# Optimization experiments

Measured on AMD Instinct MI355X. Metric: run time of the kernel, lower is better.

## Reference

```python
import jax, jax.numpy as jnp
import numpy as np

N_NODES = 50000
N_EDGES = 1600000
N_FEAT = 128
DROPOUT = 0.1


def setup_inputs() -> dict:
    key = jax.random.key(0)
    k1, k2, k3, k4 = jax.random.split(key, 4)
    x = jax.random.normal(k1, (N_NODES, N_FEAT), dtype=jnp.float32)
    adj_vals = jax.random.uniform(k2, (N_EDGES,), dtype=jnp.float32)
    row = jax.random.randint(k3, (N_EDGES,), 0, N_NODES, dtype=jnp.int32)
    col = jax.random.randint(k4, (N_EDGES,), 0, N_NODES, dtype=jnp.int32)
    return {"x": x, "adj_vals": adj_vals, "row": row, "col": col}


def reference(x, adj_vals, row, col):
    # MixedDropout on sparse adjacency values (deterministic fixed key),
    # then SpMM: out[i] = sum_{e: row[e]==i} A_drop[e] * x[col[e]]
    keep_prob = 1.0 - DROPOUT
    mask_key = jax.random.fold_in(jax.random.key(42), 7)
    keep = jax.random.bernoulli(mask_key, keep_prob, adj_vals.shape)
    vals_drop = jnp.where(keep, adj_vals / keep_prob, 0.0)
    # gather source features and weight by (dropped) edge values
    msgs = vals_drop[:, None] * x[col]  # [E, F]
    out = jax.ops.segment_sum(msgs, row, num_segments=N_NODES)  # [N, F]
    return out
```

## Files before the change

kernel.cpp:

```cpp
#include <hip/hip_runtime.h>
#include <stdint.h>

#define N_NODES 50000
#define N_EDGES 1600000
#define N_FEAT 128
#define CAP 64
#define OVF_PW 256
#define OVF_PB 192

#define RSHIFT 7
#define BROWS 128
#define NB 391
#define NWG_A 250
#define A_THREADS 1024
#define CHUNKS_PW 1600
#define CAPW 40
#define NREG (NWG_A + NB)


struct KeyPair { uint32_t a, b; };

__host__ __device__ constexpr inline uint32_t rotl32(uint32_t x, int r) {
  return (x << r) | (x >> (32 - r));
}

__host__ __device__ constexpr inline KeyPair threefry2x32(uint32_t k0, uint32_t k1,
                                                          uint32_t x0, uint32_t x1) {
  const uint32_t ks0 = k0, ks1 = k1, ks2 = k0 ^ k1 ^ 0x1BD11BDAu;
  x0 += ks0;
  x1 += ks1;
  const int rotA[4] = {13, 15, 26, 6};
  const int rotB[4] = {17, 29, 16, 24};
  const uint32_t ks[3] = {ks0, ks1, ks2};
  for (int i = 0; i < 5; ++i) {
    const int* rot = (i & 1) ? rotB : rotA;
    for (int j = 0; j < 4; ++j) {
      x0 += x1;
      x1 = rotl32(x1, rot[j]);
      x1 ^= x0;
    }
    x0 += ks[(i + 1) % 3];
    x1 += ks[(i + 2) % 3] + (uint32_t)(i + 1);
  }
  return {x0, x1};
}

constexpr KeyPair MASK_KEY = threefry2x32(0u, 42u, 0u, 7u);

__device__ inline bool edge_keep(uint32_t e) {
  KeyPair r = threefry2x32(MASK_KEY.a, MASK_KEY.b, 0u, e);
  uint32_t bits = r.a ^ r.b;
  float u = __uint_as_float((bits >> 9) | 0x3f800000u) - 1.0f;
  return u < 0.9f;
}

__device__ inline uint32_t f2bf(uint32_t b) {
  return (b + 0x7fffu + ((b >> 16) & 1u)) >> 16;
}

typedef uint32_t u4v __attribute__((ext_vector_type(4)));
typedef int32_t  i4v __attribute__((ext_vector_type(4)));
typedef float    f4v __attribute__((ext_vector_type(4)));


__global__ void __launch_bounds__(A_THREADS) convA_kernel(const float* __restrict__ x,
                                                          uint32_t* __restrict__ xb,
                                                          const float* __restrict__ adj_vals,
                                                          const int* __restrict__ row,
                                                          const int* __restrict__ col,
                                                          uint64_t* __restrict__ coarse,
                                                          uint32_t* __restrict__ lens,
                                                          uint32_t* __restrict__ ovfcA,
                                                          uint64_t* __restrict__ ovfA) {
  __shared__ uint32_t cnt[NB];
  __shared__ uint32_t ovfc;
  int wg = blockIdx.x;
  int tid = threadIdx.x;
  if (tid < NB) cnt[tid] = 0;
  if (tid == 0) ovfc = 0;

  const int gthreads = NWG_A * A_THREADS;
  for (int i = wg * A_THREADS + tid; i < (N_NODES * N_FEAT) / 8; i += gthreads) {
    f4v a = __builtin_nontemporal_load((const f4v*)x + 2 * i);
    f4v b = __builtin_nontemporal_load((const f4v*)x + 2 * i + 1);
    u4v o;
    o.x = f2bf(__float_as_uint(a.x)) | (f2bf(__float_as_uint(a.y)) << 16);
    o.y = f2bf(__float_as_uint(a.z)) | (f2bf(__float_as_uint(a.w)) << 16);
    o.z = f2bf(__float_as_uint(b.x)) | (f2bf(__float_as_uint(b.y)) << 16);
    o.w = f2bf(__float_as_uint(b.z)) | (f2bf(__float_as_uint(b.w)) << 16);
    ((u4v*)xb)[i] = o;
  }
  __syncthreads();

  uint64_t* my_coarse = coarse + (size_t)wg * NB * CAPW;
  for (int ch = tid; ch < CHUNKS_PW; ch += A_THREADS) {
    const int g = wg * CHUNKS_PW + ch;
    const i4v r4 = __builtin_nontemporal_load((const i4v*)row + g);
    const i4v c4 = __builtin_nontemporal_load((const i4v*)col + g);
    const f4v a4 = __builtin_nontemporal_load((const f4v*)adj_vals + g);
    const int rr[4] = {r4.x, r4.y, r4.z, r4.w};
    const int cc[4] = {c4.x, c4.y, c4.z, c4.w};
    const float aa[4] = {a4.x, a4.y, a4.z, a4.w};
#pragma unroll
    for (int k = 0; k < 4; ++k) {
      const uint32_t e = (uint32_t)(4 * g + k);
      if (!edge_keep(e)) continue;
      const uint32_t r = (uint32_t)rr[k];
      const uint32_t c = (uint32_t)cc[k];
      const float v = aa[k] / 0.9f;
      const uint32_t b = r >> RSHIFT;
      const uint32_t li = atomicAdd(&cnt[b], 1u);
      const uint64_t p = ((uint64_t)r << 48) | ((uint64_t)c << 32) | (uint64_t)__float_as_uint(v);
      if (li < CAPW) {
        my_coarse[(size_t)b * CAPW + li] = p;
      } else {
        const uint32_t oi = atomicAdd(&ovfc, 1u);
        if (oi < OVF_PW) ovfA[(size_t)wg * OVF_PW + oi] = p;
      }
    }
  }
  __syncthreads();
  if (tid < NB) lens[(size_t)tid * NWG_A + wg] = min(cnt[tid], (uint32_t)CAPW);
  if (tid == 0) ovfcA[wg] = min(ovfc, (uint32_t)OVF_PW);
}

__global__ void __launch_bounds__(512) rank_gather_kernel(const uint32_t* __restrict__ xb,
                                                          const uint64_t* __restrict__ coarse,
                                                          const uint32_t* __restrict__ lens,
                                                          uint32_t* __restrict__ ovfcB,
                                                          uint64_t* __restrict__ ovfB,
                                                          float* __restrict__ out) {
  int b = blockIdx.x;
  int tid = threadIdx.x;
  __shared__ uint32_t pay[BROWS * CAP];
  __shared__ uint32_t cnt[BROWS];
  __shared__ uint32_t s_len[NWG_A];
  __shared__ uint32_t ovfc;
  for (int i = tid; i < BROWS * CAP; i += 512) pay[i] = 0u;
  if (tid < BROWS) cnt[tid] = 0;
  if (tid < NWG_A) s_len[tid] = lens[(size_t)b * NWG_A + tid];
  if (tid == 0) ovfc = 0;
  __syncthreads();

  int team = tid >> 4;
  int lane = tid & 15;

  uint32_t lenv[8];
  uint64_t pre[8];
#pragma unroll
  for (int s8 = 0; s8 < 8; ++s8) {
    int seg = team + (s8 << 5);
    lenv[s8] = (seg < NWG_A) ? s_len[seg] : 0u;
    pre[s8] = (seg < NWG_A)
        ? __builtin_nontemporal_load(coarse + ((size_t)seg * NB + b) * CAPW + lane)
        : 0ull;
  }
  uint64_t tl[8];
#pragma unroll
  for (int s8 = 0; s8 < 8; ++s8) {
    int seg = team + (s8 << 5);
    tl[s8] = (lenv[s8] > 16u && (uint32_t)(lane + 16) < lenv[s8])
        ? __builtin_nontemporal_load(coarse + ((size_t)seg * NB + b) * CAPW + 16 + lane)
        : 0ull;
  }

#define RANK(p)                                                              \
  {                                                                          \
    uint32_t r = (uint32_t)((p) >> 48);                                      \
    uint32_t rl = r & (BROWS - 1);                                           \
    uint32_t idx = atomicAdd(&cnt[rl], 1u);                                  \
    if (idx < CAP) {                                                         \
      uint32_t c = (uint32_t)((p) >> 32) & 0xFFFFu;                          \
      pay[rl * CAP + idx] = (c << 16) | f2bf((uint32_t)(p));                 \
    } else {                                                                 \
      uint32_t oi = atomicAdd(&ovfc, 1u);                                    \
      if (oi < OVF_PB) ovfB[(size_t)b * OVF_PB + oi] = (p);                  \
    }                                                                        \
  }

#pragma unroll
  for (int s8 = 0; s8 < 8; ++s8) {
    if ((uint32_t)lane < lenv[s8]) RANK(pre[s8]);
  }
#pragma unroll
  for (int s8 = 0; s8 < 8; ++s8) {
    if (lenv[s8] > 16u && (uint32_t)(lane + 16) < lenv[s8]) RANK(tl[s8]);
  }
#pragma unroll
  for (int s8 = 0; s8 < 8; ++s8) {
    uint32_t len = lenv[s8];
    if (len > 32u) {
      int seg = team + (s8 << 5);
      const uint64_t* cseg = coarse + ((size_t)seg * NB + b) * CAPW;
      for (uint32_t li = 32u + (uint32_t)lane; li < len; li += 16) {
        uint64_t p = __builtin_nontemporal_load(cseg + li);
        RANK(p);
      }
    }
  }
#undef RANK
  __syncthreads();
  if (tid == 0) ovfcB[b] = min(ovfc, (uint32_t)OVF_PB);

  const uint4* x4 = (const uint4*)xb;
  const int r0 = b << RSHIFT;

#define GSTEP(ww)                                                            \
  {                                                                          \
    uint32_t cc = (ww) >> 16;                                                \
    float vv = __uint_as_float((ww) << 16);                                  \
    uint4 a = x4[(size_t)cc * 16 + lane];                                    \
    acc0 += vv * __uint_as_float(a.x << 16);                                 \
    acc1 += vv * __uint_as_float(a.x & 0xffff0000u);                         \
    acc2 += vv * __uint_as_float(a.y << 16);                                 \
    acc3 += vv * __uint_as_float(a.y & 0xffff0000u);                         \
    acc4 += vv * __uint_as_float(a.z << 16);                                 \
    acc5 += vv * __uint_as_float(a.z & 0xffff0000u);                         \
    acc6 += vv * __uint_as_float(a.w << 16);                                 \
    acc7 += vv * __uint_as_float(a.w & 0xffff0000u);                         \
  }

  for (int rl = team; rl < BROWS; rl += 32) {
    int r = r0 + rl;
    if (r >= N_NODES) continue;
    uint32_t n = (min(cnt[rl], (uint32_t)CAP) + 7u) & ~7u;
    const uint32_t* prow = &pay[rl * CAP];
    float acc0 = 0.f, acc1 = 0.f, acc2 = 0.f, acc3 = 0.f;
    float acc4 = 0.f, acc5 = 0.f, acc6 = 0.f, acc7 = 0.f;
    for (uint32_t j = 0; j < n; j += 8) {
      uint32_t w0 = prow[j + 0];
      uint32_t w1 = prow[j + 1];
      uint32_t w2 = prow[j + 2];
      uint32_t w3 = prow[j + 3];
      uint32_t w4 = prow[j + 4];
      uint32_t w5 = prow[j + 5];
      uint32_t w6 = prow[j + 6];
      uint32_t w7 = prow[j + 7];
      GSTEP(w0) GSTEP(w1) GSTEP(w2) GSTEP(w3)
      GSTEP(w4) GSTEP(w5) GSTEP(w6) GSTEP(w7)
    }
    f4v lo, hi;
    lo.x = acc0; lo.y = acc1; lo.z = acc2; lo.w = acc3;
    hi.x = acc4; hi.y = acc5; hi.z = acc6; hi.w = acc7;
    f4v* o = (f4v*)out + (size_t)r * 32 + lane * 2;
    __builtin_nontemporal_store(lo, o);
    __builtin_nontemporal_store(hi, o + 1);
  }
#undef GSTEP
}

__global__ void __launch_bounds__(256) ovf_pack_kernel(const float* __restrict__ x,
                                                       const uint32_t* __restrict__ ovfcA,
                                                       const uint64_t* __restrict__ ovfA,
                                                       const uint32_t* __restrict__ ovfcB,
                                                       const uint64_t* __restrict__ ovfB,
                                                       float* __restrict__ out) {
  __shared__ int any;
  if (threadIdx.x == 0) any = 0;
  __syncthreads();
  for (int t = threadIdx.x; t < NREG; t += 256) {
    uint32_t c = (t < NWG_A) ? ovfcA[t] : ovfcB[t - NWG_A];
    if (c) any = 1;
  }
  __syncthreads();
  if (!any) return;

  int group = (int)((blockIdx.x * 256 + threadIdx.x) >> 7);
  int f = threadIdx.x & 127;
  const int ngroups = (16 * 256) >> 7;
  for (int reg = group; reg < NREG; reg += ngroups) {
    uint32_t c;
    const uint64_t* basep;
    if (reg < NWG_A) {
      c = min(ovfcA[reg], (uint32_t)OVF_PW);
      basep = ovfA + (size_t)reg * OVF_PW;
    } else {
      c = min(ovfcB[reg - NWG_A], (uint32_t)OVF_PB);
      basep = ovfB + (size_t)(reg - NWG_A) * OVF_PB;
    }
    for (uint32_t i = 0; i < c; ++i) {
      uint64_t p = basep[i];
      uint32_t r = (uint32_t)(p >> 48);
      uint32_t cc = (uint32_t)((p >> 32) & 0xFFFFu);
      float v = __uint_as_float((uint32_t)p);
      atomicAdd(&out[(size_t)r * N_FEAT + f], v * x[(size_t)cc * N_FEAT + f]);
    }
  }
}


__global__ void __launch_bounds__(256) scatter_fused_kernel(const float* __restrict__ x,
                                                            const float* __restrict__ adj_vals,
                                                            const int* __restrict__ row,
                                                            const int* __restrict__ col,
                                                            float* __restrict__ out) {
  long long t = (long long)blockIdx.x * blockDim.x + threadIdx.x;
  int e = (int)(t >> 6);
  int lane = (int)(t & 63);
  if (e >= N_EDGES) return;
  if (!edge_keep((uint32_t)e)) return;
  float v = adj_vals[e] / 0.9f;
  float2 xf = *(const float2*)(x + (long long)col[e] * N_FEAT + lane * 2);
  float* dst = out + (long long)row[e] * N_FEAT + lane * 2;
  atomicAdd(dst, v * xf.x);
  atomicAdd(dst + 1, v * xf.y);
}


extern "C" void kernel_launch(void* const* d_in, const int* in_sizes, int n_in,
                              void* d_out, int out_size, void* d_ws, size_t ws_size,
                              hipStream_t stream) {
  const float* x        = (const float*)d_in[0];
  const float* adj_vals = (const float*)d_in[1];
  const int*   row      = (const int*)d_in[2];
  const int*   col      = (const int*)d_in[3];
  float* out = (float*)d_out;

  size_t a_ovfcA   = 0;
  size_t a_ovfcB   = (a_ovfcA + (size_t)NWG_A * 4 + 255) & ~255ull;
  size_t a_lens    = (a_ovfcB + (size_t)NB * 4 + 255) & ~255ull;
  size_t a_ovfA    = (a_lens + (size_t)NB * NWG_A * 4 + 255) & ~255ull;
  size_t a_ovfB    = (a_ovfA + (size_t)NWG_A * OVF_PW * 8 + 255) & ~255ull;
  size_t a_coarse  = (a_ovfB + (size_t)NB * OVF_PB * 8 + 255) & ~255ull;
  size_t a_xb      = (a_coarse + (size_t)NWG_A * NB * CAPW * 8 + 255) & ~255ull;
  size_t need      = a_xb + (size_t)N_NODES * N_FEAT * 2;

  if (ws_size >= need) {
    uint32_t* ovfcA   = (uint32_t*)((char*)d_ws + a_ovfcA);
    uint32_t* ovfcB   = (uint32_t*)((char*)d_ws + a_ovfcB);
    uint32_t* lens    = (uint32_t*)((char*)d_ws + a_lens);
    uint64_t* ovfA    = (uint64_t*)((char*)d_ws + a_ovfA);
    uint64_t* ovfB    = (uint64_t*)((char*)d_ws + a_ovfB);
    uint64_t* coarse  = (uint64_t*)((char*)d_ws + a_coarse);
    uint32_t* xb      = (uint32_t*)((char*)d_ws + a_xb);

    convA_kernel<<<NWG_A, A_THREADS, 0, stream>>>(x, xb, adj_vals, row, col,
                                                  coarse, lens, ovfcA, ovfA);
    rank_gather_kernel<<<NB, 512, 0, stream>>>(xb, coarse, lens, ovfcB, ovfB, out);
    ovf_pack_kernel<<<16, 256, 0, stream>>>(x, ovfcA, ovfA, ovfcB, ovfB, out);
  } else {
    hipMemsetAsync(d_out, 0, (size_t)out_size * sizeof(float), stream);
    long long total_threads = (long long)N_EDGES * 64;
    scatter_fused_kernel<<<(int)((total_threads + 255) / 256), 256, 0, stream>>>(
        x, adj_vals, row, col, out);
  }
}
```

Measured before the change: 152.1 us.

## Split coarse bucket records into packed payload and row-local byte arrays

The binning pass now writes each edge as a 32-bit packed column/bf16 value word plus a separate 8-bit local row index, instead of one 64-bit record. The bf16 conversion moves out of the ranking kernel, which shrinks both the intermediate write and its later re-read. The ranking kernel also rotates slot indices by the local row to spread LDS bank accesses, and the overflow buffer becomes 32-bit with a repacked encoding. The extra byte-array loads are narrow and may coalesce poorly, and the sync moved ahead of the x conversion loop changes where the block waits.

```diff
diff --git a/kernel.cpp b/kernel.cpp
--- a/kernel.cpp
+++ b/kernel.cpp
@@ -68,7 +68,8 @@
                                                           const float* __restrict__ adj_vals,
                                                           const int* __restrict__ row,
                                                           const int* __restrict__ col,
-                                                          uint64_t* __restrict__ coarse,
+                                                          uint32_t* __restrict__ cpay,
+                                                          uint8_t* __restrict__ crl,
                                                           uint32_t* __restrict__ lens,
                                                           uint32_t* __restrict__ ovfcA,
                                                           uint64_t* __restrict__ ovfA) {
@@ -78,6 +79,7 @@
   int tid = threadIdx.x;
   if (tid < NB) cnt[tid] = 0;
   if (tid == 0) ovfc = 0;
+  __syncthreads();
 
   const int gthreads = NWG_A * A_THREADS;
   for (int i = wg * A_THREADS + tid; i < (N_NODES * N_FEAT) / 8; i += gthreads) {
@@ -90,9 +92,9 @@
     o.w = f2bf(__float_as_uint(b.z)) | (f2bf(__float_as_uint(b.w)) << 16);
     ((u4v*)xb)[i] = o;
   }
-  __syncthreads();
-
-  uint64_t* my_coarse = coarse + (size_t)wg * NB * CAPW;
+
+  uint32_t* my_pay = cpay + (size_t)wg * NB * CAPW;
+  uint8_t* my_rl = crl + (size_t)wg * NB * CAPW;
   for (int ch = tid; ch < CHUNKS_PW; ch += A_THREADS) {
     const int g = wg * CHUNKS_PW + ch;
     const i4v r4 = __builtin_nontemporal_load((const i4v*)row + g);
@@ -110,12 +112,15 @@
       const float v = aa[k] / 0.9f;
       const uint32_t b = r >> RSHIFT;
       const uint32_t li = atomicAdd(&cnt[b], 1u);
-      const uint64_t p = ((uint64_t)r << 48) | ((uint64_t)c << 32) | (uint64_t)__float_as_uint(v);
       if (li < CAPW) {
-        my_coarse[(size_t)b * CAPW + li] = p;
+        const size_t off = (size_t)b * CAPW + li;
+        my_pay[off] = (c << 16) | f2bf(__float_as_uint(v));
+        my_rl[off] = (uint8_t)(r & (BROWS - 1));
       } else {
         const uint32_t oi = atomicAdd(&ovfc, 1u);
-        if (oi < OVF_PW) ovfA[(size_t)wg * OVF_PW + oi] = p;
+        if (oi < OVF_PW)
+          ovfA[(size_t)wg * OVF_PW + oi] =
+              ((uint64_t)r << 48) | ((uint64_t)c << 32) | (uint64_t)__float_as_uint(v);
       }
     }
   }
@@ -125,10 +130,11 @@
 }
 
 __global__ void __launch_bounds__(512) rank_gather_kernel(const uint32_t* __restrict__ xb,
-                                                          const uint64_t* __restrict__ coarse,
+                                                          const uint32_t* __restrict__ cpay,
+                                                          const uint8_t* __restrict__ crl,
                                                           const uint32_t* __restrict__ lens,
                                                           uint32_t* __restrict__ ovfcB,
-                                                          uint64_t* __restrict__ ovfB,
+                                                          uint32_t* __restrict__ ovfB,
                                                           float* __restrict__ out) {
   int b = blockIdx.x;
   int tid = threadIdx.x;
@@ -146,55 +152,56 @@
   int lane = tid & 15;
 
   uint32_t lenv[8];
-  uint64_t pre[8];
+  uint32_t pw[8];
+  uint32_t prl[8];
 #pragma unroll
   for (int s8 = 0; s8 < 8; ++s8) {
     int seg = team + (s8 << 5);
     lenv[s8] = (seg < NWG_A) ? s_len[seg] : 0u;
-    pre[s8] = (seg < NWG_A)
-        ? __builtin_nontemporal_load(coarse + ((size_t)seg * NB + b) * CAPW + lane)
-        : 0ull;
-  }
-  uint64_t tl[8];
+    size_t off = ((size_t)seg * NB + b) * CAPW + lane;
+    pw[s8] = (seg < NWG_A) ? __builtin_nontemporal_load(cpay + off) : 0u;
+    prl[s8] = (seg < NWG_A) ? (uint32_t)__builtin_nontemporal_load(crl + off) : 0u;
+  }
+  uint32_t tw[8];
+  uint32_t trl[8];
 #pragma unroll
   for (int s8 = 0; s8 < 8; ++s8) {
     int seg = team + (s8 << 5);
-    tl[s8] = (lenv[s8] > 16u && (uint32_t)(lane + 16) < lenv[s8])
-        ? __builtin_nontemporal_load(coarse + ((size_t)seg * NB + b) * CAPW + 16 + lane)
-        : 0ull;
-  }
-
-#define RANK(p)                                                              \
+    bool tv = (lenv[s8] > 16u && (uint32_t)(lane + 16) < lenv[s8]);
+    size_t off = ((size_t)seg * NB + b) * CAPW + 16 + lane;
+    tw[s8] = tv ? __builtin_nontemporal_load(cpay + off) : 0u;
+    trl[s8] = tv ? (uint32_t)__builtin_nontemporal_load(crl + off) : 0u;
+  }
+
+#define RANK(w, rl)                                                          \
   {                                                                          \
-    uint32_t r = (uint32_t)((p) >> 48);                                      \
-    uint32_t rl = r & (BROWS - 1);                                           \
-    uint32_t idx = atomicAdd(&cnt[rl], 1u);                                  \
+    uint32_t idx = atomicAdd(&cnt[(rl)], 1u);                                \
     if (idx < CAP) {                                                         \
-      uint32_t c = (uint32_t)((p) >> 32) & 0xFFFFu;                          \
-      pay[rl * CAP + idx] = (c << 16) | f2bf((uint32_t)(p));                 \
+      pay[(rl) * CAP + ((idx + (rl)) & (CAP - 1))] = (w);                    \
     } else {                                                                 \
       uint32_t oi = atomicAdd(&ovfc, 1u);                                    \
-      if (oi < OVF_PB) ovfB[(size_t)b * OVF_PB + oi] = (p);                  \
+      if (oi < OVF_PB) ovfB[(size_t)b * OVF_PB + oi] = ((rl) << 24) | ((w) >> 8) | (((w) & 0xFFu) << 16); \
     }                                                                        \
   }
 
 #pragma unroll
   for (int s8 = 0; s8 < 8; ++s8) {
-    if ((uint32_t)lane < lenv[s8]) RANK(pre[s8]);
-  }
-#pragma unroll
-  for (int s8 = 0; s8 < 8; ++s8) {
-    if (lenv[s8] > 16u && (uint32_t)(lane + 16) < lenv[s8]) RANK(tl[s8]);
+    if ((uint32_t)lane < lenv[s8]) RANK(pw[s8], prl[s8]);
+  }
+#pragma unroll
+  for (int s8 = 0; s8 < 8; ++s8) {
+    if (lenv[s8] > 16u && (uint32_t)(lane + 16) < lenv[s8]) RANK(tw[s8], trl[s8]);
   }
 #pragma unroll
   for (int s8 = 0; s8 < 8; ++s8) {
     uint32_t len = lenv[s8];
     if (len > 32u) {
       int seg = team + (s8 << 5);
-      const uint64_t* cseg = coarse + ((size_t)seg * NB + b) * CAPW;
+      size_t sbase = ((size_t)seg * NB + b) * CAPW;
       for (uint32_t li = 32u + (uint32_t)lane; li < len; li += 16) {
-        uint64_t p = __builtin_nontemporal_load(cseg + li);
-        RANK(p);
+        uint32_t w = __builtin_nontemporal_load(cpay + sbase + li);
+        uint32_t rl = (uint32_t)__builtin_nontemporal_load(crl + sbase + li);
+        RANK(w, rl);
       }
     }
   }
@@ -228,14 +235,14 @@
     float acc0 = 0.f, acc1 = 0.f, acc2 = 0.f, acc3 = 0.f;
     float acc4 = 0.f, acc5 = 0.f, acc6 = 0.f, acc7 = 0.f;
     for (uint32_t j = 0; j < n; j += 8) {
-      uint32_t w0 = prow[j + 0];
-      uint32_t w1 = prow[j + 1];
-      uint32_t w2 = prow[j + 2];
-      uint32_t w3 = prow[j + 3];
-      uint32_t w4 = prow[j + 4];
-      uint32_t w5 = prow[j + 5];
-      uint32_t w6 = prow[j + 6];
-      uint32_t w7 = prow[j + 7];
+      uint32_t w0 = prow[(j + 0 + rl) & (CAP - 1)];
+      uint32_t w1 = prow[(j + 1 + rl) & (CAP - 1)];
+      uint32_t w2 = prow[(j + 2 + rl) & (CAP - 1)];
+      uint32_t w3 = prow[(j + 3 + rl) & (CAP - 1)];
+      uint32_t w4 = prow[(j + 4 + rl) & (CAP - 1)];
+      uint32_t w5 = prow[(j + 5 + rl) & (CAP - 1)];
+      uint32_t w6 = prow[(j + 6 + rl) & (CAP - 1)];
+      uint32_t w7 = prow[(j + 7 + rl) & (CAP - 1)];
       GSTEP(w0) GSTEP(w1) GSTEP(w2) GSTEP(w3)
       GSTEP(w4) GSTEP(w5) GSTEP(w6) GSTEP(w7)
     }
@@ -253,13 +260,13 @@
                                                        const uint32_t* __restrict__ ovfcA,
                                                        const uint64_t* __restrict__ ovfA,
                                                        const uint32_t* __restrict__ ovfcB,
-                                                       const uint64_t* __restrict__ ovfB,
+                                                       const uint32_t* __restrict__ ovfB,
                                                        float* __restrict__ out) {
   __shared__ int any;
   if (threadIdx.x == 0) any = 0;
   __syncthreads();
   for (int t = threadIdx.x; t < NREG; t += 256) {
-    uint32_t c = (t < NWG_A) ? ovfcA[t] : ovfcB[t - NWG_A];
+    uint32_t c = (t < NWG_A) ? ovfcA[t] : ovfcB ? ((t - NWG_A < NB) ? ovfcB[t - NWG_A] : 0u) : 0u;
     if (c) any = 1;
   }
   __syncthreads();
@@ -269,21 +276,29 @@
   int f = threadIdx.x & 127;
   const int ngroups = (16 * 256) >> 7;
   for (int reg = group; reg < NREG; reg += ngroups) {
-    uint32_t c;
-    const uint64_t* basep;
     if (reg < NWG_A) {
-      c = min(ovfcA[reg], (uint32_t)OVF_PW);
-      basep = ovfA + (size_t)reg * OVF_PW;
+      uint32_t c = min(ovfcA[reg], (uint32_t)OVF_PW);
+      const uint64_t* basep = ovfA + (size_t)reg * OVF_PW;
+      for (uint32_t i = 0; i < c; ++i) {
+        uint64_t p = basep[i];
+        uint32_t r = (uint32_t)(p >> 48);
+        uint32_t cc = (uint32_t)((p >> 32) & 0xFFFFu);
+        float v = __uint_as_float((uint32_t)p);
+        atomicAdd(&out[(size_t)r * N_FEAT + f], v * x[(size_t)cc * N_FEAT + f]);
+      }
     } else {
-      c = min(ovfcB[reg - NWG_A], (uint32_t)OVF_PB);
-      basep = ovfB + (size_t)(reg - NWG_A) * OVF_PB;
-    }
-    for (uint32_t i = 0; i < c; ++i) {
-      uint64_t p = basep[i];
-      uint32_t r = (uint32_t)(p >> 48);
-      uint32_t cc = (uint32_t)((p >> 32) & 0xFFFFu);
-      float v = __uint_as_float((uint32_t)p);
-      atomicAdd(&out[(size_t)r * N_FEAT + f], v * x[(size_t)cc * N_FEAT + f]);
+      int bb = reg - NWG_A;
+      uint32_t c = min(ovfcB[bb], (uint32_t)OVF_PB);
+      const uint32_t* basep = ovfB + (size_t)bb * OVF_PB;
+      for (uint32_t i = 0; i < c; ++i) {
+        uint32_t s = basep[i];
+        uint32_t rl = s >> 24;
+        uint32_t w = ((s & 0x00FFFFu) << 8) | ((s >> 16) & 0xFFu);
+        uint32_t r = ((uint32_t)bb << RSHIFT) + rl;
+        uint32_t cc = w >> 16;
+        float v = __uint_as_float(w << 16);
+        atomicAdd(&out[(size_t)r * N_FEAT + f], v * x[(size_t)cc * N_FEAT + f]);
+      }
     }
   }
 }
@@ -321,22 +336,24 @@
   size_t a_lens    = (a_ovfcB + (size_t)NB * 4 + 255) & ~255ull;
   size_t a_ovfA    = (a_lens + (size_t)NB * NWG_A * 4 + 255) & ~255ull;
   size_t a_ovfB    = (a_ovfA + (size_t)NWG_A * OVF_PW * 8 + 255) & ~255ull;
-  size_t a_coarse  = (a_ovfB + (size_t)NB * OVF_PB * 8 + 255) & ~255ull;
-  size_t a_xb      = (a_coarse + (size_t)NWG_A * NB * CAPW * 8 + 255) & ~255ull;
+  size_t a_cpay    = (a_ovfB + (size_t)NB * OVF_PB * 4 + 255) & ~255ull;
+  size_t a_crl     = (a_cpay + (size_t)NWG_A * NB * CAPW * 4 + 255) & ~255ull;
+  size_t a_xb      = (a_crl + (size_t)NWG_A * NB * CAPW + 255) & ~255ull;
   size_t need      = a_xb + (size_t)N_NODES * N_FEAT * 2;
 
   if (ws_size >= need) {
-    uint32_t* ovfcA   = (uint32_t*)((char*)d_ws + a_ovfcA);
-    uint32_t* ovfcB   = (uint32_t*)((char*)d_ws + a_ovfcB);
-    uint32_t* lens    = (uint32_t*)((char*)d_ws + a_lens);
-    uint64_t* ovfA    = (uint64_t*)((char*)d_ws + a_ovfA);
-    uint64_t* ovfB    = (uint64_t*)((char*)d_ws + a_ovfB);
-    uint64_t* coarse  = (uint64_t*)((char*)d_ws + a_coarse);
-    uint32_t* xb      = (uint32_t*)((char*)d_ws + a_xb);
+    uint32_t* ovfcA = (uint32_t*)((char*)d_ws + a_ovfcA);
+    uint32_t* ovfcB = (uint32_t*)((char*)d_ws + a_ovfcB);
+    uint32_t* lens  = (uint32_t*)((char*)d_ws + a_lens);
+    uint64_t* ovfA  = (uint64_t*)((char*)d_ws + a_ovfA);
+    uint32_t* ovfB  = (uint32_t*)((char*)d_ws + a_ovfB);
+    uint32_t* cpay  = (uint32_t*)((char*)d_ws + a_cpay);
+    uint8_t*  crl   = (uint8_t*)((char*)d_ws + a_crl);
+    uint32_t* xb    = (uint32_t*)((char*)d_ws + a_xb);
 
     convA_kernel<<<NWG_A, A_THREADS, 0, stream>>>(x, xb, adj_vals, row, col,
-                                                  coarse, lens, ovfcA, ovfA);
-    rank_gather_kernel<<<NB, 512, 0, stream>>>(xb, coarse, lens, ovfcB, ovfB, out);
+                                                  cpay, crl, lens, ovfcA, ovfA);
+    rank_gather_kernel<<<NB, 512, 0, stream>>>(xb, cpay, crl, lens, ovfcB, ovfB, out);
     ovf_pack_kernel<<<16, 256, 0, stream>>>(x, ovfcA, ovfA, ovfcB, ovfB, out);
   } else {
     hipMemsetAsync(d_out, 0, (size_t)out_size * sizeof(float), stream);
```

After: 158.1 us. +4.0%, slower.

## Halve row buckets to 64 rows, rotate LDS slots, move barrier earlier

Applied to the files above, without the earlier changes.

Buckets now cover 64 rows instead of 128, which doubles the number of rank/gather workgroups, shrinks each workgroup to 256 threads and shrinks the per-workgroup coarse capacity and overflow budget. The LDS payload slot index is rotated by the row index so concurrent reads and writes across teams spread over banks. The barrier in convA now sits right after the shared counters are cleared, so the bf16 conversion loop and edge bucketing are no longer separated by a sync. The aim is more parallelism and less LDS per block. The smaller per-bucket capacity may push more edges to the overflow path.

```diff
diff --git a/kernel.cpp b/kernel.cpp
--- a/kernel.cpp
+++ b/kernel.cpp
@@ -6,15 +6,15 @@
 #define N_FEAT 128
 #define CAP 64
 #define OVF_PW 256
-#define OVF_PB 192
-
-#define RSHIFT 7
-#define BROWS 128
-#define NB 391
+#define OVF_PB 128
+
+#define RSHIFT 6
+#define BROWS 64
+#define NB 782
 #define NWG_A 250
 #define A_THREADS 1024
 #define CHUNKS_PW 1600
-#define CAPW 40
+#define CAPW 24
 #define NREG (NWG_A + NB)
 
 
@@ -78,6 +78,7 @@
   int tid = threadIdx.x;
   if (tid < NB) cnt[tid] = 0;
   if (tid == 0) ovfc = 0;
+  __syncthreads();
 
   const int gthreads = NWG_A * A_THREADS;
   for (int i = wg * A_THREADS + tid; i < (N_NODES * N_FEAT) / 8; i += gthreads) {
@@ -90,7 +91,6 @@
     o.w = f2bf(__float_as_uint(b.z)) | (f2bf(__float_as_uint(b.w)) << 16);
     ((u4v*)xb)[i] = o;
   }
-  __syncthreads();
 
   uint64_t* my_coarse = coarse + (size_t)wg * NB * CAPW;
   for (int ch = tid; ch < CHUNKS_PW; ch += A_THREADS) {
@@ -124,7 +124,7 @@
   if (tid == 0) ovfcA[wg] = min(ovfc, (uint32_t)OVF_PW);
 }
 
-__global__ void __launch_bounds__(512) rank_gather_kernel(const uint32_t* __restrict__ xb,
+__global__ void __launch_bounds__(256) rank_gather_kernel(const uint32_t* __restrict__ xb,
                                                           const uint64_t* __restrict__ coarse,
                                                           const uint32_t* __restrict__ lens,
                                                           uint32_t* __restrict__ ovfcB,
@@ -136,7 +136,7 @@
   __shared__ uint32_t cnt[BROWS];
   __shared__ uint32_t s_len[NWG_A];
   __shared__ uint32_t ovfc;
-  for (int i = tid; i < BROWS * CAP; i += 512) pay[i] = 0u;
+  for (int i = tid; i < BROWS * CAP; i += 256) pay[i] = 0u;
   if (tid < BROWS) cnt[tid] = 0;
   if (tid < NWG_A) s_len[tid] = lens[(size_t)b * NWG_A + tid];
   if (tid == 0) ovfc = 0;
@@ -145,22 +145,14 @@
   int team = tid >> 4;
   int lane = tid & 15;
 
-  uint32_t lenv[8];
-  uint64_t pre[8];
+  uint32_t lenv[16];
+  uint64_t pre[16];
 #pragma unroll
-  for (int s8 = 0; s8 < 8; ++s8) {
-    int seg = team + (s8 << 5);
-    lenv[s8] = (seg < NWG_A) ? s_len[seg] : 0u;
-    pre[s8] = (seg < NWG_A)
+  for (int s = 0; s < 16; ++s) {
+    int seg = team + (s << 4);
+    lenv[s] = (seg < NWG_A) ? s_len[seg] : 0u;
+    pre[s] = (seg < NWG_A)
         ? __builtin_nontemporal_load(coarse + ((size_t)seg * NB + b) * CAPW + lane)
-        : 0ull;
-  }
-  uint64_t tl[8];
-#pragma unroll
-  for (int s8 = 0; s8 < 8; ++s8) {
-    int seg = team + (s8 << 5);
-    tl[s8] = (lenv[s8] > 16u && (uint32_t)(lane + 16) < lenv[s8])
-        ? __builtin_nontemporal_load(coarse + ((size_t)seg * NB + b) * CAPW + 16 + lane)
         : 0ull;
   }
 
@@ -171,7 +163,7 @@
     uint32_t idx = atomicAdd(&cnt[rl], 1u);                                  \
     if (idx < CAP) {                                                         \
       uint32_t c = (uint32_t)((p) >> 32) & 0xFFFFu;                          \
-      pay[rl * CAP + idx] = (c << 16) | f2bf((uint32_t)(p));                 \
+      pay[rl * CAP + ((idx + rl) & (CAP - 1))] = (c << 16) | f2bf((uint32_t)(p)); \
     } else {                                                                 \
       uint32_t oi = atomicAdd(&ovfc, 1u);                                    \
       if (oi < OVF_PB) ovfB[(size_t)b * OVF_PB + oi] = (p);                  \
@@ -179,20 +171,16 @@
   }
 
 #pragma unroll
-  for (int s8 = 0; s8 < 8; ++s8) {
-    if ((uint32_t)lane < lenv[s8]) RANK(pre[s8]);
+  for (int s = 0; s < 16; ++s) {
+    if ((uint32_t)lane < lenv[s]) RANK(pre[s]);
   }
 #pragma unroll
-  for (int s8 = 0; s8 < 8; ++s8) {
-    if (lenv[s8] > 16u && (uint32_t)(lane + 16) < lenv[s8]) RANK(tl[s8]);
-  }
-#pragma unroll
-  for (int s8 = 0; s8 < 8; ++s8) {
-    uint32_t len = lenv[s8];
-    if (len > 32u) {
-      int seg = team + (s8 << 5);
+  for (int s = 0; s < 16; ++s) {
+    uint32_t len = lenv[s];
+    if (len > 16u) {
+      int seg = team + (s << 4);
       const uint64_t* cseg = coarse + ((size_t)seg * NB + b) * CAPW;
-      for (uint32_t li = 32u + (uint32_t)lane; li < len; li += 16) {
+      for (uint32_t li = 16u + (uint32_t)lane; li < len; li += 16) {
         uint64_t p = __builtin_nontemporal_load(cseg + li);
         RANK(p);
       }
@@ -220,7 +208,7 @@
     acc7 += vv * __uint_as_float(a.w & 0xffff0000u);                         \
   }
 
-  for (int rl = team; rl < BROWS; rl += 32) {
+  for (int rl = team; rl < BROWS; rl += 16) {
     int r = r0 + rl;
     if (r >= N_NODES) continue;
     uint32_t n = (min(cnt[rl], (uint32_t)CAP) + 7u) & ~7u;
@@ -228,14 +216,14 @@
     float acc0 = 0.f, acc1 = 0.f, acc2 = 0.f, acc3 = 0.f;
     float acc4 = 0.f, acc5 = 0.f, acc6 = 0.f, acc7 = 0.f;
     for (uint32_t j = 0; j < n; j += 8) {
-      uint32_t w0 = prow[j + 0];
-      uint32_t w1 = prow[j + 1];
-      uint32_t w2 = prow[j + 2];
-      uint32_t w3 = prow[j + 3];
-      uint32_t w4 = prow[j + 4];
-      uint32_t w5 = prow[j + 5];
-      uint32_t w6 = prow[j + 6];
-      uint32_t w7 = prow[j + 7];
+      uint32_t w0 = prow[(j + 0 + rl) & (CAP - 1)];
+      uint32_t w1 = prow[(j + 1 + rl) & (CAP - 1)];
+      uint32_t w2 = prow[(j + 2 + rl) & (CAP - 1)];
+      uint32_t w3 = prow[(j + 3 + rl) & (CAP - 1)];
+      uint32_t w4 = prow[(j + 4 + rl) & (CAP - 1)];
+      uint32_t w5 = prow[(j + 5 + rl) & (CAP - 1)];
+      uint32_t w6 = prow[(j + 6 + rl) & (CAP - 1)];
+      uint32_t w7 = prow[(j + 7 + rl) & (CAP - 1)];
       GSTEP(w0) GSTEP(w1) GSTEP(w2) GSTEP(w3)
       GSTEP(w4) GSTEP(w5) GSTEP(w6) GSTEP(w7)
     }
@@ -326,17 +314,17 @@
   size_t need      = a_xb + (size_t)N_NODES * N_FEAT * 2;
 
   if (ws_size >= need) {
-    uint32_t* ovfcA   = (uint32_t*)((char*)d_ws + a_ovfcA);
-    uint32_t* ovfcB   = (uint32_t*)((char*)d_ws + a_ovfcB);
-    uint32_t* lens    = (uint32_t*)((char*)d_ws + a_lens);
-    uint64_t* ovfA    = (uint64_t*)((char*)d_ws + a_ovfA);
-    uint64_t* ovfB    = (uint64_t*)((char*)d_ws + a_ovfB);
-    uint64_t* coarse  = (uint64_t*)((char*)d_ws + a_coarse);
-    uint32_t* xb      = (uint32_t*)((char*)d_ws + a_xb);
+    uint32_t* ovfcA = (uint32_t*)((char*)d_ws + a_ovfcA);
+    uint32_t* ovfcB = (uint32_t*)((char*)d_ws + a_ovfcB);
+    uint32_t* lens  = (uint32_t*)((char*)d_ws + a_lens);
+    uint64_t* ovfA  = (uint64_t*)((char*)d_ws + a_ovfA);
+    uint64_t* ovfB  = (uint64_t*)((char*)d_ws + a_ovfB);
+    uint64_t* coarse = (uint64_t*)((char*)d_ws + a_coarse);
+    uint32_t* xb    = (uint32_t*)((char*)d_ws + a_xb);
 
     convA_kernel<<<NWG_A, A_THREADS, 0, stream>>>(x, xb, adj_vals, row, col,
                                                   coarse, lens, ovfcA, ovfA);
-    rank_gather_kernel<<<NB, 512, 0, stream>>>(xb, coarse, lens, ovfcB, ovfB, out);
+    rank_gather_kernel<<<NB, 256, 0, stream>>>(xb, coarse, lens, ovfcB, ovfB, out);
     ovf_pack_kernel<<<16, 256, 0, stream>>>(x, ovfcA, ovfA, ovfcB, ovfB, out);
   } else {
     hipMemsetAsync(d_out, 0, (size_t)out_size * sizeof(float), stream);
```

Result: slower. 161.7 us (+6.3%).

## Transpose coarse bucket layout to bucket-major and rotate LDS payload slots per row

Applied to the files above, without the earlier changes.

The coarse staging buffer becomes bucket-major ([bucket][workgroup][slot]) instead of workgroup-major, so each rank_gather block reads one contiguous region rather than 250 strided segments. Payload slots in LDS are rotated by the row index, which spreads the gather-loop reads of different rows across LDS banks. The barrier after zeroing the shared counters moves to before the bf16 conversion loop, so the bucketing phase no longer waits on it. In exchange, the scattered writes in convA become more spread across memory.

```diff
diff --git a/kernel.cpp b/kernel.cpp
--- a/kernel.cpp
+++ b/kernel.cpp
@@ -78,6 +78,7 @@
   int tid = threadIdx.x;
   if (tid < NB) cnt[tid] = 0;
   if (tid == 0) ovfc = 0;
+  __syncthreads();
 
   const int gthreads = NWG_A * A_THREADS;
   for (int i = wg * A_THREADS + tid; i < (N_NODES * N_FEAT) / 8; i += gthreads) {
@@ -90,9 +91,7 @@
     o.w = f2bf(__float_as_uint(b.z)) | (f2bf(__float_as_uint(b.w)) << 16);
     ((u4v*)xb)[i] = o;
   }
-  __syncthreads();
-
-  uint64_t* my_coarse = coarse + (size_t)wg * NB * CAPW;
+
   for (int ch = tid; ch < CHUNKS_PW; ch += A_THREADS) {
     const int g = wg * CHUNKS_PW + ch;
     const i4v r4 = __builtin_nontemporal_load((const i4v*)row + g);
@@ -112,7 +111,7 @@
       const uint32_t li = atomicAdd(&cnt[b], 1u);
       const uint64_t p = ((uint64_t)r << 48) | ((uint64_t)c << 32) | (uint64_t)__float_as_uint(v);
       if (li < CAPW) {
-        my_coarse[(size_t)b * CAPW + li] = p;
+        coarse[((size_t)b * NWG_A + wg) * CAPW + li] = p;
       } else {
         const uint32_t oi = atomicAdd(&ovfc, 1u);
         if (oi < OVF_PW) ovfA[(size_t)wg * OVF_PW + oi] = p;
@@ -144,6 +143,7 @@
 
   int team = tid >> 4;
   int lane = tid & 15;
+  const uint64_t* cbase = coarse + (size_t)b * NWG_A * CAPW;
 
   uint32_t lenv[8];
   uint64_t pre[8];
@@ -152,16 +152,15 @@
     int seg = team + (s8 << 5);
     lenv[s8] = (seg < NWG_A) ? s_len[seg] : 0u;
     pre[s8] = (seg < NWG_A)
-        ? __builtin_nontemporal_load(coarse + ((size_t)seg * NB + b) * CAPW + lane)
+        ? __builtin_nontemporal_load(cbase + (size_t)seg * CAPW + lane)
         : 0ull;
   }
   uint64_t tl[8];
 #pragma unroll
   for (int s8 = 0; s8 < 8; ++s8) {
     int seg = team + (s8 << 5);
-    tl[s8] = (lenv[s8] > 16u && (uint32_t)(lane + 16) < lenv[s8])
-        ? __builtin_nontemporal_load(coarse + ((size_t)seg * NB + b) * CAPW + 16 + lane)
-        : 0ull;
+    bool tv = (lenv[s8] > 16u && (uint32_t)(lane + 16) < lenv[s8]);
+    tl[s8] = tv ? __builtin_nontemporal_load(cbase + (size_t)seg * CAPW + 16 + lane) : 0ull;
   }
 
 #define RANK(p)                                                              \
@@ -171,7 +170,7 @@
     uint32_t idx = atomicAdd(&cnt[rl], 1u);                                  \
     if (idx < CAP) {                                                         \
       uint32_t c = (uint32_t)((p) >> 32) & 0xFFFFu;                          \
-      pay[rl * CAP + idx] = (c << 16) | f2bf((uint32_t)(p));                 \
+      pay[rl * CAP + ((idx + rl) & (CAP - 1))] = (c << 16) | f2bf((uint32_t)(p)); \
     } else {                                                                 \
       uint32_t oi = atomicAdd(&ovfc, 1u);                                    \
       if (oi < OVF_PB) ovfB[(size_t)b * OVF_PB + oi] = (p);                  \
@@ -191,7 +190,7 @@
     uint32_t len = lenv[s8];
     if (len > 32u) {
       int seg = team + (s8 << 5);
-      const uint64_t* cseg = coarse + ((size_t)seg * NB + b) * CAPW;
+      const uint64_t* cseg = cbase + (size_t)seg * CAPW;
       for (uint32_t li = 32u + (uint32_t)lane; li < len; li += 16) {
         uint64_t p = __builtin_nontemporal_load(cseg + li);
         RANK(p);
@@ -228,14 +227,14 @@
     float acc0 = 0.f, acc1 = 0.f, acc2 = 0.f, acc3 = 0.f;
     float acc4 = 0.f, acc5 = 0.f, acc6 = 0.f, acc7 = 0.f;
     for (uint32_t j = 0; j < n; j += 8) {
-      uint32_t w0 = prow[j + 0];
-      uint32_t w1 = prow[j + 1];
-      uint32_t w2 = prow[j + 2];
-      uint32_t w3 = prow[j + 3];
-      uint32_t w4 = prow[j + 4];
-      uint32_t w5 = prow[j + 5];
-      uint32_t w6 = prow[j + 6];
-      uint32_t w7 = prow[j + 7];
+      uint32_t w0 = prow[(j + 0 + rl) & (CAP - 1)];
+      uint32_t w1 = prow[(j + 1 + rl) & (CAP - 1)];
+      uint32_t w2 = prow[(j + 2 + rl) & (CAP - 1)];
+      uint32_t w3 = prow[(j + 3 + rl) & (CAP - 1)];
+      uint32_t w4 = prow[(j + 4 + rl) & (CAP - 1)];
+      uint32_t w5 = prow[(j + 5 + rl) & (CAP - 1)];
+      uint32_t w6 = prow[(j + 6 + rl) & (CAP - 1)];
+      uint32_t w7 = prow[(j + 7 + rl) & (CAP - 1)];
       GSTEP(w0) GSTEP(w1) GSTEP(w2) GSTEP(w3)
       GSTEP(w4) GSTEP(w5) GSTEP(w6) GSTEP(w7)
     }
@@ -322,17 +321,17 @@
   size_t a_ovfA    = (a_lens + (size_t)NB * NWG_A * 4 + 255) & ~255ull;
   size_t a_ovfB    = (a_ovfA + (size_t)NWG_A * OVF_PW * 8 + 255) & ~255ull;
   size_t a_coarse  = (a_ovfB + (size_t)NB * OVF_PB * 8 + 255) & ~255ull;
-  size_t a_xb      = (a_coarse + (size_t)NWG_A * NB * CAPW * 8 + 255) & ~255ull;
+  size_t a_xb      = (a_coarse + (size_t)NB * NWG_A * CAPW * 8 + 255) & ~255ull;
   size_t need      = a_xb + (size_t)N_NODES * N_FEAT * 2;
 
   if (ws_size >= need) {
-    uint32_t* ovfcA   = (uint32_t*)((char*)d_ws + a_ovfcA);
-    uint32_t* ovfcB   = (uint32_t*)((char*)d_ws + a_ovfcB);
-    uint32_t* lens    = (uint32_t*)((char*)d_ws + a_lens);
-    uint64_t* ovfA    = (uint64_t*)((char*)d_ws + a_ovfA);
-    uint64_t* ovfB    = (uint64_t*)((char*)d_ws + a_ovfB);
-    uint64_t* coarse  = (uint64_t*)((char*)d_ws + a_coarse);
-    uint32_t* xb      = (uint32_t*)((char*)d_ws + a_xb);
+    uint32_t* ovfcA = (uint32_t*)((char*)d_ws + a_ovfcA);
+    uint32_t* ovfcB = (uint32_t*)((char*)d_ws + a_ovfcB);
+    uint32_t* lens  = (uint32_t*)((char*)d_ws + a_lens);
+    uint64_t* ovfA  = (uint64_t*)((char*)d_ws + a_ovfA);
+    uint64_t* ovfB  = (uint64_t*)((char*)d_ws + a_ovfB);
+    uint64_t* coarse = (uint64_t*)((char*)d_ws + a_coarse);
+    uint32_t* xb    = (uint32_t*)((char*)d_ws + a_xb);
 
     convA_kernel<<<NWG_A, A_THREADS, 0, stream>>>(x, xb, adj_vals, row, col,
                                                   coarse, lens, ovfcA, ovfA);
```

After: 153.4 us. Within noise of the previous version (+0.9%).
